# Kernel optimization log

Hardware: AMD Instinct MI355X
Metric: run time of the kernel (lower is better)

Reference implementation:

```python
import jax, jax.numpy as jnp
import numpy as np
from functools import partial

IM = 1280            # input image side
VAR = (0.1, 0.2)     # retinaface variances
TOPK = 1024          # pre-NMS candidates per image
CONF_T = 0.5         # confidence threshold
NMS_T = 0.4          # IoU threshold
MIN_SIZES = [[16, 32], [64, 128], [256, 512]]
STEPS = [8, 16, 32]


def make_priors():
    """Vectorized PriorBox for a 1280x1280 image -> [A,4] (cx,cy,w,h), normalized."""
    chunks = []
    for ms_list, step in zip(MIN_SIZES, STEPS):
        f = IM // step
        c = (np.arange(f, dtype=np.float32) + 0.5) * step / IM
        cy, cx = np.meshgrid(c, c, indexing='ij')
        for ms in ms_list:
            s = np.float32(ms) / IM
            a = np.stack([cx, cy, np.full_like(cx, s), np.full_like(cx, s)], -1)
            chunks.append(a.reshape(-1, 4))
    return np.concatenate(chunks, 0)  # [67200, 4]


def setup_inputs() -> dict:
    key = jax.random.key(0)
    k1, k2, k3 = jax.random.split(key, 3)
    N, A = 32, 67200
    return {
        "loc": jax.random.normal(k1, (N, A, 4), jnp.float32),
        "conf": jax.random.normal(k2, (N, A, 2), jnp.float32),
        "landms": jax.random.normal(k3, (N, A, 10), jnp.float32),
        "priors": jnp.asarray(make_priors()),
    }


def _pairwise_iou(boxes):
    # boxes: [K,4] corner format
    x1 = jnp.maximum(boxes[:, None, 0], boxes[None, :, 0])
    y1 = jnp.maximum(boxes[:, None, 1], boxes[None, :, 1])
    x2 = jnp.minimum(boxes[:, None, 2], boxes[None, :, 2])
    y2 = jnp.minimum(boxes[:, None, 3], boxes[None, :, 3])
    inter = jnp.clip(x2 - x1, 0.0) * jnp.clip(y2 - y1, 0.0)
    area = jnp.clip(boxes[:, 2] - boxes[:, 0], 0.0) * jnp.clip(boxes[:, 3] - boxes[:, 1], 0.0)
    return inter / (area[:, None] + area[None, :] - inter + 1e-9)


def _nms_one(boxes, scores):
    # greedy NMS over score-sorted candidates (boxes already sorted desc by score)
    K = boxes.shape[0]
    iou = _pairwise_iou(boxes)                 # [K,K]
    idx = jnp.arange(K)
    valid = scores > CONF_T

    def body(i, keep):
        sup = (iou[i] > NMS_T) & keep[i] & (idx > i)
        return keep & ~sup

    return jax.lax.fori_loop(0, K, body, valid)


def reference(loc, conf, landms, priors):
    N, A, _ = loc.shape
    # softmax face scores
    scores = jax.nn.softmax(conf, axis=-1)[..., 1]                       # [N,A]
    # decode boxes (variances 0.1 / 0.2)
    cxcy = priors[None, :, :2] + loc[..., :2] * VAR[0] * priors[None, :, 2:]
    wh = priors[None, :, 2:] * jnp.exp(loc[..., 2:] * VAR[1])
    boxes = jnp.concatenate([cxcy - wh * 0.5, cxcy + wh * 0.5], -1) * IM  # [N,A,4]
    # decode 5 landmarks
    lm = landms.reshape(N, A, 5, 2)
    pts = (priors[None, :, None, :2] + lm * VAR[0] * priors[None, :, None, 2:]) * IM
    pts = pts.reshape(N, A, 10)                                          # [N,A,10]
    # top-K candidates per image (sorted by score, descending)
    top_s, top_i = jax.lax.top_k(scores, TOPK)                           # [N,K]
    gb = jnp.take_along_axis(boxes, top_i[..., None], axis=1)            # [N,K,4]
    gl = jnp.take_along_axis(pts, top_i[..., None], axis=1)              # [N,K,10]
    keep = jax.vmap(_nms_one)(gb, top_s)                                 # [N,K] bool
    det = jnp.concatenate([gb, top_s[..., None], gl], -1)                # [N,K,15]
    return det * keep[..., None].astype(det.dtype)
```

## Files before the change

### kernel.cpp

```cpp
#include <hip/hip_runtime.h>

typedef unsigned int u32;
typedef unsigned long long u64;

#define N_IMG 32
#define NA 67200
#define KTOP 1024
#define IM_F 1280.0f
#define HBLK 16
#define CHUNK 4200
#define SEGCAP 768
#define ECAP 256
#define PRETHR 0x3F666666u

__device__ __forceinline__ float cr_expf(float x) { return (float)exp((double)x); }

__device__ __forceinline__ u64 shflxor64(u64 v, int m) {
    u32 lo = (u32)__shfl_xor((int)(u32)v, m, 64);
    u32 hi = (u32)__shfl_xor((int)(u32)(v >> 32), m, 64);
    return ((u64)hi << 32) | (u64)lo;
}

__device__ __forceinline__ u64 readlane64(u64 v, int lane) {
    u32 lo = (u32)__builtin_amdgcn_readlane((int)(u32)v, lane);
    u32 hi = (u32)__builtin_amdgcn_readlane((int)(u32)(v >> 32), lane);
    return ((u64)hi << 32) | (u64)lo;
}

__device__ __forceinline__ float face_score(float c0, float c1) {
    if (c1 >= c0) {
        float e0 = cr_expf(c0 - c1);
        return 1.0f / (e0 + 1.0f);
    } else {
        float e1 = cr_expf(c1 - c0);
        return e1 / (1.0f + e1);
    }
}

__global__ __launch_bounds__(256) void score_compact_kernel(const float4* __restrict__ conf4,
                                                            u64* __restrict__ keys,
                                                            u32* __restrict__ cnts) {
    const int n = blockIdx.x >> 4, blk = blockIdx.x & 15;
    const int tid = threadIdx.x;
    __shared__ u64 kbuf[SEGCAP];
    __shared__ u32 cnt;
    if (tid == 0) cnt = 0;
    __syncthreads();
    const int base2 = (n * NA + blk * CHUNK) >> 1;
    #pragma unroll 1
    for (int it = 0; it < 9; ++it) {
        const int idx = tid + it * 256;
        if (idx < CHUNK / 2) {
            float4 c = conf4[base2 + idx];
            float s0 = face_score(c.x, c.y);
            float s1 = face_score(c.z, c.w);
            u32 u0 = __float_as_uint(s0), u1 = __float_as_uint(s1);
            u32 a0 = (u32)(blk * CHUNK + idx * 2);
            if (u0 > PRETHR) {
                u32 p = atomicAdd(&cnt, 1u);
                if (p < SEGCAP) kbuf[p] = ((u64)u0 << 32) | (u32)(~a0);
            }
            if (u1 > PRETHR) {
                u32 p = atomicAdd(&cnt, 1u);
                if (p < SEGCAP) kbuf[p] = ((u64)u1 << 32) | (u32)(~(a0 + 1u));
            }
        }
    }
    __syncthreads();
    const u32 c_ = min(cnt, (u32)SEGCAP);
    u64* seg = keys + ((size_t)n * HBLK + blk) * SEGCAP;
    for (u32 i = tid; i < c_; i += 256) seg[i] = kbuf[i];
    if (tid == 0) cnts[n * HBLK + blk] = c_;
}

__global__ __launch_bounds__(1024) void select_sort_kernel(const u64* __restrict__ keys,
                                                           const u32* __restrict__ cnts,
                                                           u32* __restrict__ top_idx,
                                                           float* __restrict__ top_score) {
    const int n = blockIdx.x, tid = threadIdx.x;
    __shared__ u32 hist[4096];
    __shared__ u32 sA[1024], sB[1024];
    __shared__ u64 cand[KTOP];
    __shared__ u64 bkeys[ECAP];
    __shared__ u32 sc[4];
    for (int i = tid; i < 4096; i += 1024) hist[i] = 0;
    if (tid < 4) sc[tid] = 0;
    __syncthreads();

    const u64* kb = keys + (size_t)n * HBLK * SEGCAP;
    u32 cl[HBLK];
    #pragma unroll
    for (int b = 0; b < HBLK; ++b) cl[b] = cnts[n * HBLK + b];

    #pragma unroll 1
    for (int b = 0; b < HBLK; ++b) {
        const u64* seg = kb + b * SEGCAP;
        for (u32 i = tid; i < cl[b]; i += 1024) {
            u32 u = (u32)(seg[i] >> 32);
            u32 bin = min((u - 0x3F600000u) >> 9, 4095u);
            atomicAdd(&hist[bin], 1u);
        }
    }
    __syncthreads();

    const uint4 hv = *(const uint4*)(hist + tid * 4);
    const u32 h0 = hv.x, h1 = hv.y, h2 = hv.z, h3 = hv.w;
    sA[tid] = h0 + h1 + h2 + h3;
    __syncthreads();
    u32 *src = sA, *dst = sB;
    for (int d = 1; d < 1024; d <<= 1) {
        dst[tid] = src[tid] + ((tid + d < 1024) ? src[tid + d] : 0u);
        __syncthreads();
        u32* t = src; src = dst; dst = t;
    }
    u32 GT3 = (tid + 1 < 1024) ? src[tid + 1] : 0u;
    u32 GE3 = GT3 + h3;
    u32 GE2 = GE3 + h2;
    u32 GE1 = GE2 + h1;
    u32 GE0 = GE1 + h0;
    if (GE3 >= KTOP && GT3 < KTOP) sc[0] = 4u * tid + 3u;
    if (GE2 >= KTOP && GE3 < KTOP) sc[0] = 4u * tid + 2u;
    if (GE1 >= KTOP && GE2 < KTOP) sc[0] = 4u * tid + 1u;
    if (GE0 >= KTOP && GE1 < KTOP) sc[0] = 4u * tid + 0u;
    __syncthreads();
    const u32 B = sc[0];

    #pragma unroll 1
    for (int b = 0; b < HBLK; ++b) {
        const u64* seg = kb + b * SEGCAP;
        for (u32 i = tid; i < cl[b]; i += 1024) {
            u64 k = seg[i];
            u32 u = (u32)(k >> 32);
            u32 bin = min((u - 0x3F600000u) >> 9, 4095u);
            if (bin > B) {
                u32 p = atomicAdd(&sc[1], 1u);
                cand[p] = k;
            } else if (bin == B) {
                u32 p = atomicAdd(&sc[2], 1u);
                if (p < ECAP) bkeys[p] = k;
            }
        }
    }
    __syncthreads();

    const int D = (int)sc[1];
    const int R = KTOP - D;
    const int E = min((int)sc[2], ECAP);
    for (int t = tid; t < E; t += 1024) {
        u64 k = bkeys[t];
        int rank = 0;
        for (int j = 0; j < E; ++j) rank += (bkeys[j] > k);
        if (rank < R) cand[D + rank] = k;
    }
    __syncthreads();

    u64 v = cand[tid];
    #pragma unroll
    for (int kk = 1; kk <= 10; ++kk) {
        const int k = 1 << kk;
        #pragma unroll
        for (int jj = kk - 1; jj >= 0; --jj) {
            const int j = 1 << jj;
            u64 p;
            if (j >= 64) {
                cand[tid] = v;
                __syncthreads();
                p = cand[tid ^ j];
                __syncthreads();
            } else {
                p = shflxor64(v, j);
            }
            bool keep_max = (((tid & k) == 0) == ((tid & j) == 0));
            u64 mx = v > p ? v : p;
            u64 mn = v > p ? p : v;
            v = keep_max ? mx : mn;
        }
    }

    top_idx[n * KTOP + tid]   = ~(u32)(v & 0xFFFFFFFFull);
    top_score[n * KTOP + tid] = __uint_as_float((u32)(v >> 32));
}

__global__ __launch_bounds__(256) void mask_decode_kernel(const u32* __restrict__ top_idx,
                                                          const float* __restrict__ top_score,
                                                          const float* __restrict__ loc,
                                                          const float* __restrict__ landms,
                                                          const float* __restrict__ priors,
                                                          float* __restrict__ det,
                                                          u64* __restrict__ mask) {
    const int n    = blockIdx.x & 31;
    const int sub  = blockIdx.x >> 5;
    const int wid  = threadIdx.x >> 6;
    const int lane = threadIdx.x & 63;
    const int q    = sub * 4 + wid;
    const int tid  = threadIdx.x;

    __shared__ float bx1[KTOP], by1[KTOP], bx2[KTOP], by2[KTOP], baA[KTOP];

    #pragma unroll
    for (int k = 0; k < 4; ++k) {
        const int r  = tid + k * 256;
        const int id = n * KTOP + r;
        const u32 a  = top_idx[id];
        float4 p = *(const float4*)(priors + (size_t)a * 4);
        float4 l = *(const float4*)(loc + ((size_t)n * NA + a) * 4);
        float cx = p.x + l.x * 0.1f * p.z;
        float cy = p.y + l.y * 0.1f * p.w;
        float w  = p.z * cr_expf(l.z * 0.2f);
        float h  = p.w * cr_expf(l.w * 0.2f);
        const float o0 = (cx - w * 0.5f) * IM_F;
        const float o1 = (cy - h * 0.5f) * IM_F;
        const float o2 = (cx + w * 0.5f) * IM_F;
        const float o3 = (cy + h * 0.5f) * IM_F;
        bx1[r] = o0; by1[r] = o1; bx2[r] = o2; by2[r] = o3;
        baA[r] = fmaxf(o2 - o0, 0.f) * fmaxf(o3 - o1, 0.f);

        if (sub == 0) {
            float* o = det + (size_t)id * 15;
            o[0] = o0; o[1] = o1; o[2] = o2; o[3] = o3;
            o[4] = top_score[id];
            const float* mp = landms + ((size_t)n * NA + a) * 10;
            #pragma unroll
            for (int t = 0; t < 5; ++t) {
                o[5 + 2 * t]     = (p.x + mp[2 * t]     * 0.1f * p.z) * IM_F;
                o[5 + 2 * t + 1] = (p.y + mp[2 * t + 1] * 0.1f * p.w) * IM_F;
            }
        }
    }
    __syncthreads();

    u64* mbase = mask + (size_t)n * KTOP * 16;
    #pragma unroll 1
    for (int k = 0; k < 16; ++k) {
        const int i = k * 64 + q;
        const float x1i = bx1[i], y1i = by1[i], x2i = bx2[i], y2i = by2[i], ai = baA[i];
        u64* orow = mbase + (size_t)i * 16;
        if (lane < k) orow[lane] = 0ull;
        #pragma unroll 1
        for (int w2 = k; w2 < 16; ++w2) {
            const int j = w2 * 64 + lane;
            bool bit = false;
            if (j > i) {
                float xx1 = fmaxf(x1i, bx1[j]);
                float yy1 = fmaxf(y1i, by1[j]);
                float xx2 = fminf(x2i, bx2[j]);
                float yy2 = fminf(y2i, by2[j]);
                float inter = fmaxf(xx2 - xx1, 0.f) * fmaxf(yy2 - yy1, 0.f);
                float iou = inter / (ai + baA[j] - inter + 1e-9f);
                bit = iou > 0.4f;
            }
            u64 m = __ballot(bit);
            if (lane == 0) orow[w2] = m;
        }
    }
}

__global__ __launch_bounds__(1024) void nms_out_kernel(const float* __restrict__ top_score,
                                                       const u64* __restrict__ mask,
                                                       const float* __restrict__ det,
                                                       float* __restrict__ out) {
    const int n = blockIdx.x;
    const int tid = threadIdx.x;
    __shared__ u64 lmask[512 * 16];

    const u64* mbase = mask + (size_t)n * KTOP * 16;
    u64 myw = 0;
    if (tid < 64) {
        for (int g = 0; g < 16; ++g) {
            u64 b = __ballot(top_score[n * KTOP + g * 64 + tid] > 0.5f);
            if (tid == g) myw = b;
        }
    }

    const int lane = tid & 63;
    const int w16  = lane & 15;
    const int p4   = lane >> 4;

    #pragma unroll 1
    for (int half = 0; half < 2; ++half) {
        __syncthreads();
        #pragma unroll
        for (int k = 0; k < 8; ++k) {
            int idx = tid + k * 1024;
            int r = idx >> 4, w = idx & 15;
            lmask[(r << 4) | (w ^ (r & 15))] = mbase[(size_t)half * 8192 + idx];
        }
        __syncthreads();
        if (tid < 64) {
            #pragma unroll 1
            for (int gg = 0; gg < 8; ++gg) {
                const int g = half * 8 + gg;
                const int lbase = gg * 64;
                const int rr = lbase + lane;
                u64 colw = lmask[(rr << 4) | (g ^ (rr & 15))];
                u64 kw = readlane64(myw, g);
                #pragma unroll
                for (int l = 0; l < 64; ++l) {
                    u64 rl = readlane64(colw, l);
                    kw = ((kw >> l) & 1ull) ? (kw & ~rl) : kw;
                }
                u64 acc = 0;
                #pragma unroll
                for (int k = 0; k < 16; ++k) {
                    const int r2 = lbase + p4 * 16 + k;
                    u64 row = lmask[(r2 << 4) | (w16 ^ (r2 & 15))];
                    u64 sel = (u64)0 - ((kw >> (p4 * 16 + k)) & 1ull);
                    acc |= row & sel;
                }
                acc |= shflxor64(acc, 16);
                acc |= shflxor64(acc, 32);
                myw = (lane == g) ? kw : myw;
                myw &= ~acc;
            }
        }
    }
    __syncthreads();
    if (tid < 16) lmask[tid] = myw;
    __syncthreads();

    const float* drow = det + (size_t)n * KTOP * 15;
    float* orow = out + (size_t)n * KTOP * 15;
    for (int e = tid; e < KTOP * 15; e += 1024) {
        int k = e / 15;
        float f = ((lmask[k >> 6] >> (k & 63)) & 1ull) ? 1.0f : 0.0f;
        orow[e] = drow[e] * f;
    }
}

extern "C" void kernel_launch(void* const* d_in, const int* in_sizes, int n_in,
                              void* d_out, int out_size, void* d_ws, size_t ws_size,
                              hipStream_t stream) {
    const float*  loc    = (const float*)d_in[0];
    const float4* conf4  = (const float4*)d_in[1];
    const float*  landms = (const float*)d_in[2];
    const float*  priors = (const float*)d_in[3];

    char* ws = (char*)d_ws;
    size_t off = 0;
    auto carve = [&](size_t bytes) { void* p = ws + off; off = (off + bytes + 255) & ~255ull; return p; };
    u64*    keys      = (u64*)   carve(sizeof(u64)    * (size_t)N_IMG * HBLK * SEGCAP);
    u32*    cnts      = (u32*)   carve(sizeof(u32)    * N_IMG * HBLK);
    u32*    top_idx   = (u32*)   carve(sizeof(u32)    * N_IMG * KTOP);
    float*  top_score = (float*) carve(sizeof(float)  * N_IMG * KTOP);
    float*  det       = (float*) carve(sizeof(float)  * N_IMG * KTOP * 15);
    u64*    mask      = (u64*)   carve(sizeof(u64)    * (size_t)N_IMG * KTOP * 16);

    score_compact_kernel<<<N_IMG * HBLK, 256, 0, stream>>>(conf4, keys, cnts);
    select_sort_kernel<<<N_IMG, 1024, 0, stream>>>(keys, cnts, top_idx, top_score);
    mask_decode_kernel<<<N_IMG * HBLK, 256, 0, stream>>>(top_idx, top_score, loc, landms, priors,
                                                         det, mask);
    nms_out_kernel<<<N_IMG, 1024, 0, stream>>>(top_score, mask, det, (float*)d_out);
}
```

Before: 108.7 us.

## Fuse NMS pass into mask kernel via last-block-done atomic counter

```diff
diff --git a/kernel.cpp b/kernel.cpp
--- a/kernel.cpp
+++ b/kernel.cpp
@@ -76,7 +76,8 @@
 __global__ __launch_bounds__(1024) void select_sort_kernel(const u64* __restrict__ keys,
                                                            const u32* __restrict__ cnts,
                                                            u32* __restrict__ top_idx,
-                                                           float* __restrict__ top_score) {
+                                                           float* __restrict__ top_score,
+                                                           u32* __restrict__ done) {
     const int n = blockIdx.x, tid = threadIdx.x;
     __shared__ u32 hist[4096];
     __shared__ u32 sA[1024], sB[1024];
@@ -85,6 +86,7 @@
     __shared__ u32 sc[4];
     for (int i = tid; i < 4096; i += 1024) hist[i] = 0;
     if (tid < 4) sc[tid] = 0;
+    if (tid == 0) done[n * 16] = 0;
     __syncthreads();
 
     const u64* kb = keys + (size_t)n * HBLK * SEGCAP;
@@ -181,13 +183,15 @@
     top_score[n * KTOP + tid] = __uint_as_float((u32)(v >> 32));
 }
 
-__global__ __launch_bounds__(256) void mask_decode_kernel(const u32* __restrict__ top_idx,
-                                                          const float* __restrict__ top_score,
-                                                          const float* __restrict__ loc,
-                                                          const float* __restrict__ landms,
-                                                          const float* __restrict__ priors,
-                                                          float* __restrict__ det,
-                                                          u64* __restrict__ mask) {
+__global__ __launch_bounds__(256) void mask_decode_nms_kernel(const u32* __restrict__ top_idx,
+                                                              const float* __restrict__ top_score,
+                                                              const float* __restrict__ loc,
+                                                              const float* __restrict__ landms,
+                                                              const float* __restrict__ priors,
+                                                              float* __restrict__ det,
+                                                              u64* __restrict__ mask,
+                                                              u32* done,
+                                                              float* __restrict__ out) {
     const int n    = blockIdx.x & 31;
     const int sub  = blockIdx.x >> 5;
     const int wid  = threadIdx.x >> 6;
@@ -195,7 +199,14 @@
     const int q    = sub * 4 + wid;
     const int tid  = threadIdx.x;
 
-    __shared__ float bx1[KTOP], by1[KTOP], bx2[KTOP], by2[KTOP], baA[KTOP];
+    __shared__ float soa[5 * KTOP];
+    __shared__ u64 keepw[16];
+    __shared__ int is_last;
+    float* bx1 = soa;
+    float* by1 = soa + KTOP;
+    float* bx2 = soa + 2 * KTOP;
+    float* by2 = soa + 3 * KTOP;
+    float* baA = soa + 4 * KTOP;
 
     #pragma unroll
     for (int k = 0; k < 4; ++k) {
@@ -253,17 +264,18 @@
             if (lane == 0) orow[w2] = m;
         }
     }
-}
-
-__global__ __launch_bounds__(1024) void nms_out_kernel(const float* __restrict__ top_score,
-                                                       const u64* __restrict__ mask,
-                                                       const float* __restrict__ det,
-                                                       float* __restrict__ out) {
-    const int n = blockIdx.x;
-    const int tid = threadIdx.x;
-    __shared__ u64 lmask[512 * 16];
-
-    const u64* mbase = mask + (size_t)n * KTOP * 16;
+    __syncthreads();
+
+    if (tid == 0) {
+        __threadfence();
+        u32 old = atomicAdd(&done[n * 16], 1u);
+        is_last = (old == 15u);
+    }
+    __syncthreads();
+    if (!is_last) return;
+    __threadfence();
+
+    u64* chunkb = (u64*)soa;
     u64 myw = 0;
     if (tid < 64) {
         for (int g = 0; g < 16; ++g) {
@@ -271,58 +283,54 @@
             if (tid == g) myw = b;
         }
     }
-
-    const int lane = tid & 63;
-    const int w16  = lane & 15;
-    const int p4   = lane >> 4;
-
-    #pragma unroll 1
-    for (int half = 0; half < 2; ++half) {
+    const int w16 = tid & 15;
+    const int p4  = (tid >> 4) & 3;
+
+    #pragma unroll 1
+    for (int c = 0; c < 8; ++c) {
         __syncthreads();
-        #pragma unroll
-        for (int k = 0; k < 8; ++k) {
-            int idx = tid + k * 1024;
-            int r = idx >> 4, w = idx & 15;
-            lmask[(r << 4) | (w ^ (r & 15))] = mbase[(size_t)half * 8192 + idx];
+        for (int t = tid; t < 2048; t += 256) {
+            int rl = t >> 4, w = t & 15;
+            chunkb[(rl << 4) | (w ^ (rl & 15))] = mbase[c * 2048 + t];
         }
         __syncthreads();
         if (tid < 64) {
             #pragma unroll 1
-            for (int gg = 0; gg < 8; ++gg) {
-                const int g = half * 8 + gg;
+            for (int gg = 0; gg < 2; ++gg) {
+                const int g = c * 2 + gg;
                 const int lbase = gg * 64;
-                const int rr = lbase + lane;
-                u64 colw = lmask[(rr << 4) | (g ^ (rr & 15))];
+                const int rr = lbase + tid;
+                u64 colw = chunkb[(rr << 4) | (g ^ (rr & 15))];
                 u64 kw = readlane64(myw, g);
                 #pragma unroll
                 for (int l = 0; l < 64; ++l) {
-                    u64 rl = readlane64(colw, l);
-                    kw = ((kw >> l) & 1ull) ? (kw & ~rl) : kw;
+                    u64 rl_ = readlane64(colw, l);
+                    kw = ((kw >> l) & 1ull) ? (kw & ~rl_) : kw;
                 }
                 u64 acc = 0;
                 #pragma unroll
-                for (int k = 0; k < 16; ++k) {
-                    const int r2 = lbase + p4 * 16 + k;
-                    u64 row = lmask[(r2 << 4) | (w16 ^ (r2 & 15))];
-                    u64 sel = (u64)0 - ((kw >> (p4 * 16 + k)) & 1ull);
+                for (int k2 = 0; k2 < 16; ++k2) {
+                    const int r2 = lbase + p4 * 16 + k2;
+                    u64 row = chunkb[(r2 << 4) | (w16 ^ (r2 & 15))];
+                    u64 sel = (u64)0 - ((kw >> (p4 * 16 + k2)) & 1ull);
                     acc |= row & sel;
                 }
                 acc |= shflxor64(acc, 16);
                 acc |= shflxor64(acc, 32);
-                myw = (lane == g) ? kw : myw;
+                myw = (tid == g) ? kw : myw;
                 myw &= ~acc;
             }
         }
     }
     __syncthreads();
-    if (tid < 16) lmask[tid] = myw;
+    if (tid < 16) keepw[tid] = myw;
     __syncthreads();
 
     const float* drow = det + (size_t)n * KTOP * 15;
     float* orow = out + (size_t)n * KTOP * 15;
-    for (int e = tid; e < KTOP * 15; e += 1024) {
+    for (int e = tid; e < KTOP * 15; e += 256) {
         int k = e / 15;
-        float f = ((lmask[k >> 6] >> (k & 63)) & 1ull) ? 1.0f : 0.0f;
+        float f = ((keepw[k >> 6] >> (k & 63)) & 1ull) ? 1.0f : 0.0f;
         orow[e] = drow[e] * f;
     }
 }
@@ -344,10 +352,10 @@
     float*  top_score = (float*) carve(sizeof(float)  * N_IMG * KTOP);
     float*  det       = (float*) carve(sizeof(float)  * N_IMG * KTOP * 15);
     u64*    mask      = (u64*)   carve(sizeof(u64)    * (size_t)N_IMG * KTOP * 16);
+    u32*    done      = (u32*)   carve(sizeof(u32)    * N_IMG * 16);
 
     score_compact_kernel<<<N_IMG * HBLK, 256, 0, stream>>>(conf4, keys, cnts);
-    select_sort_kernel<<<N_IMG, 1024, 0, stream>>>(keys, cnts, top_idx, top_score);
-    mask_decode_kernel<<<N_IMG * HBLK, 256, 0, stream>>>(top_idx, top_score, loc, landms, priors,
-                                                         det, mask);
-    nms_out_kernel<<<N_IMG, 1024, 0, stream>>>(top_score, mask, det, (float*)d_out);
-}
+    select_sort_kernel<<<N_IMG, 1024, 0, stream>>>(keys, cnts, top_idx, top_score, done);
+    mask_decode_nms_kernel<<<N_IMG * HBLK, 256, 0, stream>>>(top_idx, top_score, loc, landms,
+                                                             priors, det, mask, done, (float*)d_out);
+}
```

Measured after the change: 135.2 us. +24.4%, slower.

## Fuse top-K select/sort with box decode and IoU mask kernel

Applied to the files above, without the earlier changes.

```diff
diff --git a/kernel.cpp b/kernel.cpp
--- a/kernel.cpp
+++ b/kernel.cpp
@@ -73,16 +73,26 @@
     if (tid == 0) cnts[n * HBLK + blk] = c_;
 }
 
-__global__ __launch_bounds__(1024) void select_sort_kernel(const u64* __restrict__ keys,
+__global__ __launch_bounds__(1024) void select_mask_kernel(const u64* __restrict__ keys,
                                                            const u32* __restrict__ cnts,
-                                                           u32* __restrict__ top_idx,
-                                                           float* __restrict__ top_score) {
-    const int n = blockIdx.x, tid = threadIdx.x;
-    __shared__ u32 hist[4096];
-    __shared__ u32 sA[1024], sB[1024];
-    __shared__ u64 cand[KTOP];
-    __shared__ u64 bkeys[ECAP];
+                                                           const float* __restrict__ loc,
+                                                           const float* __restrict__ landms,
+                                                           const float* __restrict__ priors,
+                                                           float* __restrict__ top_score,
+                                                           float* __restrict__ det,
+                                                           u64* __restrict__ mask) {
+    const int n   = blockIdx.x & 31;
+    const int sub = blockIdx.x >> 5;
+    const int tid = threadIdx.x;
+
+    __shared__ __align__(16) char smem[35072];
+    u32* hist  = (u32*)smem;
+    u32* sA    = (u32*)(smem + 16384);
+    u32* sB    = (u32*)(smem + 20480);
+    u64* cand  = (u64*)(smem + 24576);
+    u64* bkeys = (u64*)(smem + 32768);
     __shared__ u32 sc[4];
+
     for (int i = tid; i < 4096; i += 1024) hist[i] = 0;
     if (tid < 4) sc[tid] = 0;
     __syncthreads();
@@ -177,58 +187,44 @@
         }
     }
 
-    top_idx[n * KTOP + tid]   = ~(u32)(v & 0xFFFFFFFFull);
-    top_score[n * KTOP + tid] = __uint_as_float((u32)(v >> 32));
-}
-
-__global__ __launch_bounds__(256) void mask_decode_kernel(const u32* __restrict__ top_idx,
-                                                          const float* __restrict__ top_score,
-                                                          const float* __restrict__ loc,
-                                                          const float* __restrict__ landms,
-                                                          const float* __restrict__ priors,
-                                                          float* __restrict__ det,
-                                                          u64* __restrict__ mask) {
-    const int n    = blockIdx.x & 31;
-    const int sub  = blockIdx.x >> 5;
-    const int wid  = threadIdx.x >> 6;
-    const int lane = threadIdx.x & 63;
-    const int q    = sub * 4 + wid;
-    const int tid  = threadIdx.x;
-
-    __shared__ float bx1[KTOP], by1[KTOP], bx2[KTOP], by2[KTOP], baA[KTOP];
-
-    #pragma unroll
-    for (int k = 0; k < 4; ++k) {
-        const int r  = tid + k * 256;
-        const int id = n * KTOP + r;
-        const u32 a  = top_idx[id];
-        float4 p = *(const float4*)(priors + (size_t)a * 4);
-        float4 l = *(const float4*)(loc + ((size_t)n * NA + a) * 4);
-        float cx = p.x + l.x * 0.1f * p.z;
-        float cy = p.y + l.y * 0.1f * p.w;
-        float w  = p.z * cr_expf(l.z * 0.2f);
-        float h  = p.w * cr_expf(l.w * 0.2f);
-        const float o0 = (cx - w * 0.5f) * IM_F;
-        const float o1 = (cy - h * 0.5f) * IM_F;
-        const float o2 = (cx + w * 0.5f) * IM_F;
-        const float o3 = (cy + h * 0.5f) * IM_F;
-        bx1[r] = o0; by1[r] = o1; bx2[r] = o2; by2[r] = o3;
-        baA[r] = fmaxf(o2 - o0, 0.f) * fmaxf(o3 - o1, 0.f);
-
-        if (sub == 0) {
-            float* o = det + (size_t)id * 15;
-            o[0] = o0; o[1] = o1; o[2] = o2; o[3] = o3;
-            o[4] = top_score[id];
-            const float* mp = landms + ((size_t)n * NA + a) * 10;
-            #pragma unroll
-            for (int t = 0; t < 5; ++t) {
-                o[5 + 2 * t]     = (p.x + mp[2 * t]     * 0.1f * p.z) * IM_F;
-                o[5 + 2 * t + 1] = (p.y + mp[2 * t + 1] * 0.1f * p.w) * IM_F;
-            }
-        }
-    }
-    __syncthreads();
-
+    const u32 a  = ~(u32)(v & 0xFFFFFFFFull);
+    const float sc_ = __uint_as_float((u32)(v >> 32));
+    float4 p = *(const float4*)(priors + (size_t)a * 4);
+    float4 l = *(const float4*)(loc + ((size_t)n * NA + a) * 4);
+    float cx = p.x + l.x * 0.1f * p.z;
+    float cy = p.y + l.y * 0.1f * p.w;
+    float w  = p.z * cr_expf(l.z * 0.2f);
+    float h  = p.w * cr_expf(l.w * 0.2f);
+    const float o0 = (cx - w * 0.5f) * IM_F;
+    const float o1 = (cy - h * 0.5f) * IM_F;
+    const float o2 = (cx + w * 0.5f) * IM_F;
+    const float o3 = (cy + h * 0.5f) * IM_F;
+
+    if (sub == 0) {
+        top_score[n * KTOP + tid] = sc_;
+        float* o = det + ((size_t)n * KTOP + tid) * 15;
+        o[0] = o0; o[1] = o1; o[2] = o2; o[3] = o3; o[4] = sc_;
+        const float* mp = landms + ((size_t)n * NA + a) * 10;
+        #pragma unroll
+        for (int t = 0; t < 5; ++t) {
+            o[5 + 2 * t]     = (p.x + mp[2 * t]     * 0.1f * p.z) * IM_F;
+            o[5 + 2 * t + 1] = (p.y + mp[2 * t + 1] * 0.1f * p.w) * IM_F;
+        }
+    }
+
+    __syncthreads();
+    float* bx1 = (float*)smem;
+    float* by1 = bx1 + KTOP;
+    float* bx2 = by1 + KTOP;
+    float* by2 = bx2 + KTOP;
+    float* baA = by2 + KTOP;
+    bx1[tid] = o0; by1[tid] = o1; bx2[tid] = o2; by2[tid] = o3;
+    baA[tid] = fmaxf(o2 - o0, 0.f) * fmaxf(o3 - o1, 0.f);
+    __syncthreads();
+
+    const int wid  = tid >> 6;
+    const int lane = tid & 63;
+    const int q    = sub * 16 + wid;
     u64* mbase = mask + (size_t)n * KTOP * 16;
     #pragma unroll 1
     for (int k = 0; k < 16; ++k) {
@@ -340,14 +336,12 @@
     auto carve = [&](size_t bytes) { void* p = ws + off; off = (off + bytes + 255) & ~255ull; return p; };
     u64*    keys      = (u64*)   carve(sizeof(u64)    * (size_t)N_IMG * HBLK * SEGCAP);
     u32*    cnts      = (u32*)   carve(sizeof(u32)    * N_IMG * HBLK);
-    u32*    top_idx   = (u32*)   carve(sizeof(u32)    * N_IMG * KTOP);
     float*  top_score = (float*) carve(sizeof(float)  * N_IMG * KTOP);
     float*  det       = (float*) carve(sizeof(float)  * N_IMG * KTOP * 15);
     u64*    mask      = (u64*)   carve(sizeof(u64)    * (size_t)N_IMG * KTOP * 16);
 
     score_compact_kernel<<<N_IMG * HBLK, 256, 0, stream>>>(conf4, keys, cnts);
-    select_sort_kernel<<<N_IMG, 1024, 0, stream>>>(keys, cnts, top_idx, top_score);
-    mask_decode_kernel<<<N_IMG * HBLK, 256, 0, stream>>>(top_idx, top_score, loc, landms, priors,
-                                                         det, mask);
+    select_mask_kernel<<<N_IMG * 4, 1024, 0, stream>>>(keys, cnts, loc, landms, priors,
+                                                       top_score, det, mask);
     nms_out_kernel<<<N_IMG, 1024, 0, stream>>>(top_score, mask, det, (float*)d_out);
 }
```

Result: slower. 117.0 us (+7.6%).
